# Optimization experiments

Hardware: AMD Instinct MI355X
Metric: run time of the kernel (lower is better)

The kernel has to match this reference:

```python
import jax, jax.numpy as jnp
import numpy as np

N = 30000      # nodes
E = 480000     # edges (before self-loops)
IN = 32        # input_dim
H = 8          # heads
C = 64         # hidden_dim (per-head out channels)
HC = H * C     # 512, concat width
L = 3          # num_layers
NEG_SLOPE = 0.2  # PyG GATConv default


def setup_inputs() -> dict:
    key = jax.random.key(0)
    ks = jax.random.split(key, 16)
    s = 0.05
    return {
        "x": jax.random.normal(ks[0], (N, IN), jnp.float32),
        "edge_index": jax.random.randint(ks[1], (2, E), 0, N, jnp.int32),
        # input projection
        "W_in": jax.random.normal(ks[2], (IN, HC), jnp.float32) * s,
        "b_in": jnp.zeros((HC,), jnp.float32),
        # stacked GATConv params (L layers)
        "W_gat": jax.random.normal(ks[3], (L, HC, HC), jnp.float32) * s,
        "att_src": jax.random.normal(ks[4], (L, H, C), jnp.float32) * s,
        "att_dst": jax.random.normal(ks[5], (L, H, C), jnp.float32) * s,
        "b_gat": jnp.zeros((L, HC), jnp.float32),
        # heads
        "W_att": jax.random.normal(ks[6], (HC, H), jnp.float32) * s,
        "b_att": jnp.zeros((H,), jnp.float32),
        "W_h1": jax.random.normal(ks[7], (HC, C), jnp.float32) * s,
        "b_h1": jnp.zeros((C,), jnp.float32),
        "W_h2": jax.random.normal(ks[8], (C, 1), jnp.float32) * s,
        "b_h2": jnp.zeros((1,), jnp.float32),
    }


def _gat_layer(h, src, dst, W, a_src, a_dst, b):
    # h: [N, HC]; src/dst: [E'] (with self-loops)
    hp = (h @ W).reshape(N, H, C)                       # per-head features
    s = jnp.einsum('nhc,hc->nh', hp, a_src)             # [N, H]
    d = jnp.einsum('nhc,hc->nh', hp, a_dst)             # [N, H]
    e = jax.nn.leaky_relu(s[src] + d[dst], NEG_SLOPE)   # [E', H]
    # segment softmax over destination neighborhoods
    m = jax.ops.segment_max(e, dst, num_segments=N)     # [N, H]
    ex = jnp.exp(e - m[dst])
    den = jax.ops.segment_sum(ex, dst, num_segments=N)
    alpha = ex / (den[dst] + 1e-16)                     # [E', H]
    msg = hp[src] * alpha[:, :, None]                   # [E', H, C]
    out = jax.ops.segment_sum(msg, dst, num_segments=N).reshape(N, HC) + b
    return out


def reference(x, edge_index, W_in, b_in, W_gat, att_src, att_dst, b_gat,
              W_att, b_att, W_h1, b_h1, W_h2, b_h2):
    # PyG GATConv adds self-loops by default
    loops = jnp.arange(N, dtype=edge_index.dtype)
    src = jnp.concatenate([edge_index[0], loops])
    dst = jnp.concatenate([edge_index[1], loops])

    h = jax.nn.relu(x @ W_in + b_in)                    # input_proj + ReLU
    for l in range(L):
        h = jax.nn.relu(_gat_layer(h, src, dst, W_gat[l], att_src[l], att_dst[l], b_gat[l]))
        # dropout is identity in eval mode
    attention_weights = jax.nn.softmax(h @ W_att + b_att, axis=1)   # [N, H]
    anomaly_scores = jax.nn.sigmoid(jax.nn.relu(h @ W_h1 + b_h1) @ W_h2 + b_h2)  # [N, 1]
    return (anomaly_scores, attention_weights)
```

## Files before the change

### kernel.cpp

```cpp
#include <hip/hip_runtime.h>
#include <hip/hip_bf16.h>
#include <math.h>

#define HCW 512
#define NHD 8
#define CCH 64

typedef unsigned short u16;
typedef unsigned int   u32;
typedef __attribute__((ext_vector_type(8))) short bf16x8;
typedef __attribute__((ext_vector_type(4))) float f32x4;

__device__ __forceinline__ float bf2f(u32 u) {
  union { float f; u32 i; } v; v.i = u << 16; return v.f;
}
__device__ __forceinline__ u16 f2bf(float f) {
  u32 x = __builtin_bit_cast(u32, f);
  return (u16)((x + 0x7fff + ((x >> 16) & 1)) >> 16);
}
__device__ __forceinline__ void gload_lds16(const void* g, void* l) {
  __builtin_amdgcn_global_load_lds(
      (const __attribute__((address_space(1))) u32*)g,
      (__attribute__((address_space(3))) u32*)l, 16, 0, 0);
}

__global__ void k_hist(const int* __restrict__ ei, int* __restrict__ deg, int E, int N) {
  int e = blockIdx.x * blockDim.x + threadIdx.x;
  if (e >= E + N) return;
  int dst = (e < E) ? ei[E + e] : (e - E);
  atomicAdd(&deg[dst], 1);
}

__global__ __launch_bounds__(256) void k_scan1(const int* __restrict__ deg, int* __restrict__ ptr,
                                               int* __restrict__ bsum, int n) {
  __shared__ int sm[256];
  int b = blockIdx.x, i = b * 256 + threadIdx.x;
  int v = (i < n) ? deg[i] : 0;
  sm[threadIdx.x] = v;
  __syncthreads();
  for (int off = 1; off < 256; off <<= 1) {
    int t = (threadIdx.x >= off) ? sm[threadIdx.x - off] : 0;
    __syncthreads();
    sm[threadIdx.x] += t;
    __syncthreads();
  }
  if (i < n) ptr[i + 1] = sm[threadIdx.x];
  if (threadIdx.x == 255) bsum[b] = sm[255];
}

__global__ __launch_bounds__(256) void k_scan2(const int* __restrict__ bsum, int* __restrict__ boff, int nb) {
  __shared__ int sm[256];
  int v = (threadIdx.x < nb) ? bsum[threadIdx.x] : 0;
  sm[threadIdx.x] = v;
  __syncthreads();
  for (int off = 1; off < 256; off <<= 1) {
    int t = (threadIdx.x >= off) ? sm[threadIdx.x - off] : 0;
    __syncthreads();
    sm[threadIdx.x] += t;
    __syncthreads();
  }
  if (threadIdx.x < nb) boff[threadIdx.x] = sm[threadIdx.x] - v;
}

__global__ __launch_bounds__(256) void k_scan3(int* __restrict__ ptr, const int* __restrict__ boff, int n) {
  int i = blockIdx.x * 256 + threadIdx.x;
  if (i == 0) ptr[0] = 0;
  if (i < n) ptr[i + 1] += boff[blockIdx.x];
}

__global__ void k_fill(const int* __restrict__ ei, const int* __restrict__ ptr,
                       int* __restrict__ cnt, int* __restrict__ csr_src, int E, int N) {
  int e = blockIdx.x * blockDim.x + threadIdx.x;
  if (e >= E + N) return;
  int src, dst;
  if (e < E) { src = ei[e]; dst = ei[E + e]; } else { src = e - E; dst = e - E; }
  int pos = ptr[dst] + atomicAdd(&cnt[dst], 1);
  csr_src[pos] = src;
}

__global__ __launch_bounds__(256) void k_wconv(const float* __restrict__ W, u16* __restrict__ Wt) {
  __shared__ float sm[32][33];
  int l = blockIdx.z;
  int k0 = blockIdx.y * 32, n0 = blockIdx.x * 32;
  const float* Wl = W + (size_t)l * HCW * HCW;
  u16* Wtl = Wt + (size_t)l * HCW * HCW;
  int tx = threadIdx.x & 31, ty = threadIdx.x >> 5;
  #pragma unroll
  for (int r = 0; r < 32; r += 8)
    sm[ty + r][tx] = Wl[(size_t)(k0 + ty + r) * HCW + n0 + tx];
  __syncthreads();
  #pragma unroll
  for (int r = 0; r < 32; r += 8)
    Wtl[(size_t)(n0 + ty + r) * HCW + k0 + tx] = f2bf(sm[tx][ty + r]);
}

__global__ __launch_bounds__(256) void k_wfconv(const float* __restrict__ W_h1,
                                                const float* __restrict__ W_att,
                                                u16* __restrict__ Wf) {
  int n = blockIdx.x;
  for (int k = threadIdx.x; k < 512; k += 256) {
    float v = 0.f;
    if (n < 64) v = W_h1[(size_t)k * 64 + n];
    else if (n < 72) v = W_att[(size_t)k * 8 + (n - 64)];
    Wf[(size_t)n * 512 + k] = f2bf(v);
  }
}

__global__ __launch_bounds__(256) void k_xconv(const float* __restrict__ x, u16* __restrict__ xb, int total) {
  int i = (blockIdx.x * 256 + threadIdx.x) * 8;
  if (i >= total) return;
  float4 a = *(const float4*)(x + i);
  float4 b = *(const float4*)(x + i + 4);
  uint4 o;
  o.x = (u32)f2bf(a.x) | ((u32)f2bf(a.y) << 16);
  o.y = (u32)f2bf(a.z) | ((u32)f2bf(a.w) << 16);
  o.z = (u32)f2bf(b.x) | ((u32)f2bf(b.y) << 16);
  o.w = (u32)f2bf(b.z) | ((u32)f2bf(b.w) << 16);
  *(uint4*)(xb + i) = o;
}

__global__ __launch_bounds__(256) void k_winconv(const float* __restrict__ W, u16* __restrict__ Wt) {
  int idx = blockIdx.x * 256 + threadIdx.x;
  int n = idx >> 5, k = idx & 31;
  Wt[idx] = f2bf(W[(size_t)k * HCW + n]);
}

__global__ __launch_bounds__(256) void k_inproj3(const u16* __restrict__ xb, const u16* __restrict__ Wt,
                                                 const float* __restrict__ b, u16* __restrict__ h, int N) {
  __shared__ u16 As[128 * 32];
  __shared__ u16 Bs[128 * 32];
  int tid = threadIdx.x, lane = tid & 63, w = tid >> 6;
  int bm = blockIdx.y * 128, bn = blockIdx.x * 128;
  #pragma unroll
  for (int it = 0; it < 4; it++) {
    int g = it * 256 + tid;
    if (g < 512) {
      int row = g >> 2, gb = g & 3, gs = gb ^ (row & 3);
      int ar = bm + row; if (ar >= N) ar = N - 1;
      gload_lds16(xb + (size_t)ar * 32 + gs * 8, &As[g * 8]);
    } else {
      int gg = g - 512;
      int row = gg >> 2, gb = gg & 3, gs = gb ^ (row & 3);
      gload_lds16(Wt + (size_t)(bn + row) * 32 + gs * 8, &Bs[gg * 8]);
    }
  }
  __syncthreads();
  bf16x8 af[2];
  #pragma unroll
  for (int i = 0; i < 2; i++) {
    int rowA = w * 32 + i * 16 + (lane & 15);
    int gA = (lane >> 4) ^ (rowA & 3);
    af[i] = *(const bf16x8*)&As[rowA * 32 + gA * 8];
  }
  f32x4 acc[2][8] = {};
  #pragma unroll
  for (int j = 0; j < 8; j++) {
    int rowB = j * 16 + (lane & 15);
    int gB = (lane >> 4) ^ (rowB & 3);
    bf16x8 bfr = *(const bf16x8*)&Bs[rowB * 32 + gB * 8];
    #pragma unroll
    for (int i = 0; i < 2; i++)
      acc[i][j] = __builtin_amdgcn_mfma_f32_16x16x32_bf16(af[i], bfr, acc[i][j], 0, 0, 0);
  }
  #pragma unroll
  for (int j = 0; j < 8; j++) {
    int col = bn + j * 16 + (lane & 15);
    float bb = b[col];
    #pragma unroll
    for (int i = 0; i < 2; i++) {
      #pragma unroll
      for (int r = 0; r < 4; r++) {
        int n = bm + w * 32 + i * 16 + (lane >> 4) * 4 + r;
        if (n < N) h[(size_t)n * HCW + col] = f2bf(fmaxf(acc[i][j][r] + bb, 0.f));
      }
    }
  }
}

__global__ __launch_bounds__(256) void k_gemm_mfma(const u16* __restrict__ A,
                                                   const u16* __restrict__ Bt,
                                                   u16* __restrict__ C,
                                                   const float* __restrict__ a_src,
                                                   const float* __restrict__ a_dst,
                                                   float* __restrict__ sarr,
                                                   float* __restrict__ darr,
                                                   int M) {
  __shared__ u16 As[128 * 64];
  __shared__ u16 Bs[128 * 64];
  int tid = threadIdx.x;
  int lane = tid & 63, w = tid >> 6;
  int wr = w >> 1, wc = w & 1;
  int bm = blockIdx.y * 128, bn = blockIdx.x * 128;
  f32x4 acc[4][4] = {};
  for (int k0 = 0; k0 < 512; k0 += 64) {
    __syncthreads();
    #pragma unroll
    for (int it = 0; it < 4; it++) {
      int g = it * 256 + tid;
      int row = g >> 3;
      int gb = g & 7;
      int gs = gb ^ (row & 7);
      int ar = bm + row; if (ar >= M) ar = M - 1;
      gload_lds16(A + (size_t)ar * HCW + k0 + gs * 8, &As[g * 8]);
      gload_lds16(Bt + (size_t)(bn + row) * HCW + k0 + gs * 8, &Bs[g * 8]);
    }
    __syncthreads();
    #pragma unroll
    for (int ks = 0; ks < 2; ks++) {
      bf16x8 af[4], bfr[4];
      #pragma unroll
      for (int f = 0; f < 4; f++) {
        int rowA = wr * 64 + f * 16 + (lane & 15);
        int gA = ((ks * 4 + (lane >> 4)) ^ (rowA & 7));
        af[f] = *(const bf16x8*)&As[rowA * 64 + gA * 8];
        int rowB = wc * 64 + f * 16 + (lane & 15);
        int gB = ((ks * 4 + (lane >> 4)) ^ (rowB & 7));
        bfr[f] = *(const bf16x8*)&Bs[rowB * 64 + gB * 8];
      }
      #pragma unroll
      for (int i = 0; i < 4; i++)
        #pragma unroll
        for (int j = 0; j < 4; j++)
          acc[i][j] = __builtin_amdgcn_mfma_f32_16x16x32_bf16(af[i], bfr[j], acc[i][j], 0, 0, 0);
    }
  }
  int gr_base = bm + wr * 64;
  int gc_base = bn + wc * 64;
  #pragma unroll
  for (int i = 0; i < 4; i++) {
    #pragma unroll
    for (int j = 0; j < 4; j++) {
      int col = gc_base + j * 16 + (lane & 15);
      #pragma unroll
      for (int r = 0; r < 4; r++) {
        int rowg = gr_base + i * 16 + (lane >> 4) * 4 + r;
        if (rowg < M) C[(size_t)rowg * HCW + col] = f2bf(acc[i][j][r]);
      }
    }
  }
  int head = (bn >> 6) + wc;
  float asv[4], adv[4];
  #pragma unroll
  for (int j = 0; j < 4; j++) {
    asv[j] = a_src[head * 64 + j * 16 + (lane & 15)];
    adv[j] = a_dst[head * 64 + j * 16 + (lane & 15)];
  }
  #pragma unroll
  for (int i = 0; i < 4; i++) {
    #pragma unroll
    for (int r = 0; r < 4; r++) {
      float sv = acc[i][0][r] * asv[0] + acc[i][1][r] * asv[1]
               + acc[i][2][r] * asv[2] + acc[i][3][r] * asv[3];
      float dv = acc[i][0][r] * adv[0] + acc[i][1][r] * adv[1]
               + acc[i][2][r] * adv[2] + acc[i][3][r] * adv[3];
      sv += __shfl_xor(sv, 1); dv += __shfl_xor(dv, 1);
      sv += __shfl_xor(sv, 2); dv += __shfl_xor(dv, 2);
      sv += __shfl_xor(sv, 4); dv += __shfl_xor(dv, 4);
      sv += __shfl_xor(sv, 8); dv += __shfl_xor(dv, 8);
      if ((lane & 15) == 0) {
        int rowg = gr_base + i * 16 + (lane >> 4) * 4 + r;
        if (rowg < M) {
          sarr[(size_t)rowg * NHD + head] = sv;
          darr[(size_t)rowg * NHD + head] = dv;
        }
      }
    }
  }
}

__global__ __launch_bounds__(256) void k_alpha(const int* __restrict__ ptr, const int* __restrict__ csr_src,
                                               const float* __restrict__ s, const float* __restrict__ d,
                                               u16* __restrict__ alpha, int N) {
  int wv = threadIdx.x >> 6, lane = threadIdx.x & 63;
  int n = blockIdx.x * 4 + wv;
  if (n >= N) return;
  int hd = lane & 7, g = lane >> 3;
  int beg = ptr[n], end = ptr[n + 1];
  float dn = d[(size_t)n * NHD + hd];
  float den = 0.f;
  for (int i = beg + g; i < end; i += 8) {
    float e = s[(size_t)csr_src[i] * NHD + hd] + dn;
    e = (e > 0.f) ? e : 0.2f * e;
    den += __expf(e);
  }
  den += __shfl_xor(den, 8);
  den += __shfl_xor(den, 16);
  den += __shfl_xor(den, 32);
  float inv = 1.f / (den + 1e-16f);
  for (int i = beg + g; i < end; i += 8) {
    float e = s[(size_t)csr_src[i] * NHD + hd] + dn;
    e = (e > 0.f) ? e : 0.2f * e;
    alpha[(size_t)i * NHD + hd] = f2bf(__expf(e) * inv);
  }
}

__global__ __launch_bounds__(256) void k_agg4(const int* __restrict__ ptr, const int* __restrict__ csr_src,
                                              const u16* __restrict__ hp, const u16* __restrict__ alpha,
                                              const float* __restrict__ bias,
                                              u16* __restrict__ hout, int N) {
  int wv = threadIdx.x >> 6, lane = threadIdx.x & 63;
  int n = blockIdx.x * 4 + wv;
  if (n >= N) return;
  int hd = lane >> 3;
  int c = lane * 8;
  int beg = ptr[n], end = ptr[n + 1];
  float acc[8] = {0.f, 0.f, 0.f, 0.f, 0.f, 0.f, 0.f, 0.f};

  int i = beg;
  for (; i + 8 <= end; i += 8) {
    int sidx[8];
    u32 aw[8];
    uint4 v[8];
    #pragma unroll
    for (int u = 0; u < 8; u++) sidx[u] = csr_src[i + u];
    #pragma unroll
    for (int u = 0; u < 8; u++) aw[u] = alpha[(size_t)(i + u) * NHD + hd];
    #pragma unroll
    for (int u = 0; u < 8; u++) v[u] = *(const uint4*)(hp + (size_t)sidx[u] * HCW + c);
    #pragma unroll
    for (int u = 0; u < 8; u++) {
      float a = bf2f(aw[u]);
      u32 w0 = v[u].x, w1 = v[u].y, w2 = v[u].z, w3 = v[u].w;
      acc[0] += a * bf2f(w0 & 0xffff); acc[1] += a * bf2f(w0 >> 16);
      acc[2] += a * bf2f(w1 & 0xffff); acc[3] += a * bf2f(w1 >> 16);
      acc[4] += a * bf2f(w2 & 0xffff); acc[5] += a * bf2f(w2 >> 16);
      acc[6] += a * bf2f(w3 & 0xffff); acc[7] += a * bf2f(w3 >> 16);
    }
  }
  for (; i < end; i++) {
    int s0 = csr_src[i];
    u32 aw = alpha[(size_t)i * NHD + hd];
    uint4 v0 = *(const uint4*)(hp + (size_t)s0 * HCW + c);
    float a = bf2f(aw);
    u32 w0 = v0.x, w1 = v0.y, w2 = v0.z, w3 = v0.w;
    acc[0] += a * bf2f(w0 & 0xffff); acc[1] += a * bf2f(w0 >> 16);
    acc[2] += a * bf2f(w1 & 0xffff); acc[3] += a * bf2f(w1 >> 16);
    acc[4] += a * bf2f(w2 & 0xffff); acc[5] += a * bf2f(w2 >> 16);
    acc[6] += a * bf2f(w3 & 0xffff); acc[7] += a * bf2f(w3 >> 16);
  }

  float4 bv0 = *(const float4*)(bias + c);
  float4 bv1 = *(const float4*)(bias + c + 4);
  float bb[8] = {bv0.x, bv0.y, bv0.z, bv0.w, bv1.x, bv1.y, bv1.z, bv1.w};
  u32 out[4];
  #pragma unroll
  for (int j = 0; j < 4; j++) {
    float o0 = fmaxf(acc[2 * j] + bb[2 * j], 0.f);
    float o1 = fmaxf(acc[2 * j + 1] + bb[2 * j + 1], 0.f);
    out[j] = (u32)f2bf(o0) | ((u32)f2bf(o1) << 16);
  }
  *(uint4*)(hout + (size_t)n * HCW + c) = make_uint4(out[0], out[1], out[2], out[3]);
}

__global__ __launch_bounds__(256) void k_final2(const u16* __restrict__ A,
                                                const u16* __restrict__ Wf,
                                                const float* __restrict__ b_att,
                                                const float* __restrict__ b_h1,
                                                const float* __restrict__ W_h2,
                                                const float* __restrict__ b_h2,
                                                float* __restrict__ anomaly, float* __restrict__ attw,
                                                int M) {
  __shared__ u16 As[128 * 64];
  __shared__ u16 Bs[80 * 64];
  __shared__ float so[4][32][84];
  int tid = threadIdx.x;
  int lane = tid & 63, w = tid >> 6;
  int bm = blockIdx.x * 128;
  f32x4 acc[2][5] = {};
  for (int k0 = 0; k0 < 512; k0 += 64) {
    __syncthreads();
    #pragma unroll
    for (int it = 0; it < 7; it++) {
      int g = it * 256 + tid;
      if (g < 1024) {
        int row = g >> 3, gb = g & 7;
        int gs = gb ^ (row & 7);
        int ar = bm + row; if (ar >= M) ar = M - 1;
        gload_lds16(A + (size_t)ar * HCW + k0 + gs * 8, &As[g * 8]);
      } else if (g < 1664) {
        int gg = g - 1024;
        int row = gg >> 3, gb = gg & 7;
        int gs = gb ^ (row & 7);
        gload_lds16(Wf + (size_t)row * 512 + k0 + gs * 8, &Bs[gg * 8]);
      }
    }
    __syncthreads();
    #pragma unroll
    for (int ks = 0; ks < 2; ks++) {
      bf16x8 af[2], bfr[5];
      #pragma unroll
      for (int i = 0; i < 2; i++) {
        int rowA = w * 32 + i * 16 + (lane & 15);
        int gA = ((ks * 4 + (lane >> 4)) ^ (rowA & 7));
        af[i] = *(const bf16x8*)&As[rowA * 64 + gA * 8];
      }
      #pragma unroll
      for (int j = 0; j < 5; j++) {
        int rowB = j * 16 + (lane & 15);
        int gB = ((ks * 4 + (lane >> 4)) ^ (rowB & 7));
        bfr[j] = *(const bf16x8*)&Bs[rowB * 64 + gB * 8];
      }
      #pragma unroll
      for (int i = 0; i < 2; i++)
        #pragma unroll
        for (int j = 0; j < 5; j++)
          acc[i][j] = __builtin_amdgcn_mfma_f32_16x16x32_bf16(af[i], bfr[j], acc[i][j], 0, 0, 0);
    }
  }
  #pragma unroll
  for (int i = 0; i < 2; i++) {
    #pragma unroll
    for (int j = 0; j < 5; j++) {
      int col = j * 16 + (lane & 15);
      #pragma unroll
      for (int r = 0; r < 4; r++) {
        int row_l = i * 16 + (lane >> 4) * 4 + r;
        so[w][row_l][col] = acc[i][j][r];
      }
    }
  }
  int row_l = lane >> 1, half = lane & 1;
  int n = bm + w * 32 + row_l;
  if (n < M) {
    float hacc = 0.f;
    #pragma unroll
    for (int kk = 0; kk < 32; kk++) {
      int cc = half * 32 + kk;
      float v = fmaxf(so[w][row_l][cc] + b_h1[cc], 0.f);
      hacc += v * W_h2[cc];
    }
    hacc += __shfl_xor(hacc, 1);
    if (half == 0) {
      anomaly[n] = 1.f / (1.f + __expf(-(hacc + b_h2[0])));
    } else {
      float lg[8];
      float mx = -1e30f;
      #pragma unroll
      for (int j = 0; j < 8; j++) {
        lg[j] = so[w][row_l][64 + j] + b_att[j];
        mx = fmaxf(mx, lg[j]);
      }
      float sum = 0.f;
      #pragma unroll
      for (int j = 0; j < 8; j++) { lg[j] = __expf(lg[j] - mx); sum += lg[j]; }
      float inv = 1.f / sum;
      #pragma unroll
      for (int j = 0; j < 8; j++) attw[(size_t)n * 8 + j] = lg[j] * inv;
    }
  }
}

extern "C" void kernel_launch(void* const* d_in, const int* in_sizes, int n_in,
                              void* d_out, int out_size, void* d_ws, size_t ws_size,
                              hipStream_t stream) {
  const float* x       = (const float*)d_in[0];
  const int*   ei      = (const int*)d_in[1];
  const float* W_in    = (const float*)d_in[2];
  const float* b_in    = (const float*)d_in[3];
  const float* W_gat   = (const float*)d_in[4];
  const float* att_src = (const float*)d_in[5];
  const float* att_dst = (const float*)d_in[6];
  const float* b_gat   = (const float*)d_in[7];
  const float* W_att   = (const float*)d_in[8];
  const float* b_att   = (const float*)d_in[9];
  const float* W_h1    = (const float*)d_in[10];
  const float* b_h1    = (const float*)d_in[11];
  const float* W_h2    = (const float*)d_in[12];
  const float* b_h2    = (const float*)d_in[13];

  const int N  = in_sizes[0] / 32;
  const int E  = in_sizes[1] / 2;
  const int ET = E + N;

  char* ws = (char*)d_ws;
  size_t off = 0;
  auto alloc = [&](size_t bytes) -> void* {
    void* p = ws + off;
    off = (off + bytes + 255) & ~(size_t)255;
    return p;
  };
  u16* h     = (u16*)alloc((size_t)N * HCW * 2);
  u16* hp    = (u16*)alloc((size_t)N * HCW * 2);
  u16* Wt    = (u16*)alloc((size_t)3 * HCW * HCW * 2);
  u16* Wf    = (u16*)alloc((size_t)80 * 512 * 2);
  u16* xb    = (u16*)alloc((size_t)N * 32 * 2);
  u16* Wtin  = (u16*)alloc((size_t)512 * 32 * 2);
  u16* alpha = (u16*)alloc((size_t)ET * NHD * 2);
  float* sarr = (float*)alloc((size_t)N * NHD * 4);
  float* darr = (float*)alloc((size_t)N * NHD * 4);
  int* deg    = (int*)alloc((size_t)N * 4);
  int* ptr    = (int*)alloc((size_t)(N + 1) * 4);
  int* cnt    = (int*)alloc((size_t)N * 4);
  int* csr    = (int*)alloc((size_t)ET * 4);
  int* bsum   = (int*)alloc((size_t)1024 * 4);
  int* boff   = (int*)alloc((size_t)1024 * 4);

  float* anomaly = (float*)d_out;
  float* attw    = (float*)d_out + N;

  hipMemsetAsync(deg, 0, (size_t)N * 4, stream);
  hipMemsetAsync(cnt, 0, (size_t)N * 4, stream);

  int gbE = (ET + 255) / 256;
  int nb  = (N + 255) / 256;
  k_hist<<<gbE, 256, 0, stream>>>(ei, deg, E, N);
  k_scan1<<<nb, 256, 0, stream>>>(deg, ptr, bsum, N);
  k_scan2<<<1, 256, 0, stream>>>(bsum, boff, nb);
  k_scan3<<<nb, 256, 0, stream>>>(ptr, boff, N);
  k_fill<<<gbE, 256, 0, stream>>>(ei, ptr, cnt, csr, E, N);

  k_wconv<<<dim3(16, 16, 3), 256, 0, stream>>>(W_gat, Wt);
  k_wfconv<<<80, 256, 0, stream>>>(W_h1, W_att, Wf);
  k_xconv<<<(N * 32 / 8 + 255) / 256, 256, 0, stream>>>(x, xb, N * 32);
  k_winconv<<<64, 256, 0, stream>>>(W_in, Wtin);
  k_inproj3<<<dim3(4, (N + 127) / 128), 256, 0, stream>>>(xb, Wtin, b_in, h, N);

  dim3 ggrid(HCW / 128, (N + 127) / 128);
  for (int l = 0; l < 3; l++) {
    k_gemm_mfma<<<ggrid, 256, 0, stream>>>(h, Wt + (size_t)l * HCW * HCW, hp,
                                           att_src + (size_t)l * NHD * CCH,
                                           att_dst + (size_t)l * NHD * CCH,
                                           sarr, darr, N);
    k_alpha<<<(N + 3) / 4, 256, 0, stream>>>(ptr, csr, sarr, darr, alpha, N);
    k_agg4<<<(N + 3) / 4, 256, 0, stream>>>(ptr, csr, hp, alpha,
                                            b_gat + (size_t)l * HCW, h, N);
  }

  k_final2<<<(N + 127) / 128, 256, 0, stream>>>(h, Wf, b_att, b_h1, W_h2, b_h2,
                                                anomaly, attw, N);
}
```

Before: 483.2 us.

## Fuse softmax into aggregation, replace scan with atomic alloc, merge prep kernels, XCD-swizzle GEMM

```diff
diff --git a/kernel.cpp b/kernel.cpp
--- a/kernel.cpp
+++ b/kernel.cpp
@@ -31,98 +31,81 @@
   atomicAdd(&deg[dst], 1);
 }
 
-__global__ __launch_bounds__(256) void k_scan1(const int* __restrict__ deg, int* __restrict__ ptr,
-                                               int* __restrict__ bsum, int n) {
-  __shared__ int sm[256];
-  int b = blockIdx.x, i = b * 256 + threadIdx.x;
-  int v = (i < n) ? deg[i] : 0;
-  sm[threadIdx.x] = v;
-  __syncthreads();
-  for (int off = 1; off < 256; off <<= 1) {
-    int t = (threadIdx.x >= off) ? sm[threadIdx.x - off] : 0;
-    __syncthreads();
-    sm[threadIdx.x] += t;
-    __syncthreads();
-  }
-  if (i < n) ptr[i + 1] = sm[threadIdx.x];
-  if (threadIdx.x == 255) bsum[b] = sm[255];
-}
-
-__global__ __launch_bounds__(256) void k_scan2(const int* __restrict__ bsum, int* __restrict__ boff, int nb) {
-  __shared__ int sm[256];
-  int v = (threadIdx.x < nb) ? bsum[threadIdx.x] : 0;
-  sm[threadIdx.x] = v;
-  __syncthreads();
-  for (int off = 1; off < 256; off <<= 1) {
-    int t = (threadIdx.x >= off) ? sm[threadIdx.x - off] : 0;
-    __syncthreads();
-    sm[threadIdx.x] += t;
-    __syncthreads();
-  }
-  if (threadIdx.x < nb) boff[threadIdx.x] = sm[threadIdx.x] - v;
-}
-
-__global__ __launch_bounds__(256) void k_scan3(int* __restrict__ ptr, const int* __restrict__ boff, int n) {
-  int i = blockIdx.x * 256 + threadIdx.x;
-  if (i == 0) ptr[0] = 0;
-  if (i < n) ptr[i + 1] += boff[blockIdx.x];
-}
-
-__global__ void k_fill(const int* __restrict__ ei, const int* __restrict__ ptr,
+__global__ __launch_bounds__(256) void k_alloc(const int* __restrict__ deg, int* __restrict__ beg,
+                                               int* __restrict__ cursor, int N) {
+  int n = blockIdx.x * 256 + threadIdx.x;
+  int lane = threadIdx.x & 63;
+  int v = (n < N) ? deg[n] : 0;
+  int incl = v;
+  #pragma unroll
+  for (int off = 1; off < 64; off <<= 1) {
+    int t = __shfl_up(incl, off);
+    if (lane >= off) incl += t;
+  }
+  int total = __shfl(incl, 63);
+  int base = 0;
+  if (lane == 63) base = atomicAdd(cursor, total);
+  base = __shfl(base, 63);
+  if (n < N) beg[n] = base + incl - v;
+}
+
+__global__ void k_fill(const int* __restrict__ ei, const int* __restrict__ beg,
                        int* __restrict__ cnt, int* __restrict__ csr_src, int E, int N) {
   int e = blockIdx.x * blockDim.x + threadIdx.x;
   if (e >= E + N) return;
   int src, dst;
   if (e < E) { src = ei[e]; dst = ei[E + e]; } else { src = e - E; dst = e - E; }
-  int pos = ptr[dst] + atomicAdd(&cnt[dst], 1);
+  int pos = beg[dst] + atomicAdd(&cnt[dst], 1);
   csr_src[pos] = src;
 }
 
-__global__ __launch_bounds__(256) void k_wconv(const float* __restrict__ W, u16* __restrict__ Wt) {
+__global__ __launch_bounds__(256) void k_prep(const float* __restrict__ W_gat, u16* __restrict__ Wt,
+                                              const float* __restrict__ W_h1, const float* __restrict__ W_att,
+                                              u16* __restrict__ Wf,
+                                              const float* __restrict__ x, u16* __restrict__ xb, int xtotal,
+                                              const float* __restrict__ W_in, u16* __restrict__ Wtin,
+                                              int XB) {
   __shared__ float sm[32][33];
-  int l = blockIdx.z;
-  int k0 = blockIdx.y * 32, n0 = blockIdx.x * 32;
-  const float* Wl = W + (size_t)l * HCW * HCW;
-  u16* Wtl = Wt + (size_t)l * HCW * HCW;
-  int tx = threadIdx.x & 31, ty = threadIdx.x >> 5;
-  #pragma unroll
-  for (int r = 0; r < 32; r += 8)
-    sm[ty + r][tx] = Wl[(size_t)(k0 + ty + r) * HCW + n0 + tx];
-  __syncthreads();
-  #pragma unroll
-  for (int r = 0; r < 32; r += 8)
-    Wtl[(size_t)(n0 + ty + r) * HCW + k0 + tx] = f2bf(sm[tx][ty + r]);
-}
-
-__global__ __launch_bounds__(256) void k_wfconv(const float* __restrict__ W_h1,
-                                                const float* __restrict__ W_att,
-                                                u16* __restrict__ Wf) {
-  int n = blockIdx.x;
-  for (int k = threadIdx.x; k < 512; k += 256) {
-    float v = 0.f;
-    if (n < 64) v = W_h1[(size_t)k * 64 + n];
-    else if (n < 72) v = W_att[(size_t)k * 8 + (n - 64)];
-    Wf[(size_t)n * 512 + k] = f2bf(v);
-  }
-}
-
-__global__ __launch_bounds__(256) void k_xconv(const float* __restrict__ x, u16* __restrict__ xb, int total) {
-  int i = (blockIdx.x * 256 + threadIdx.x) * 8;
-  if (i >= total) return;
-  float4 a = *(const float4*)(x + i);
-  float4 b = *(const float4*)(x + i + 4);
-  uint4 o;
-  o.x = (u32)f2bf(a.x) | ((u32)f2bf(a.y) << 16);
-  o.y = (u32)f2bf(a.z) | ((u32)f2bf(a.w) << 16);
-  o.z = (u32)f2bf(b.x) | ((u32)f2bf(b.y) << 16);
-  o.w = (u32)f2bf(b.z) | ((u32)f2bf(b.w) << 16);
-  *(uint4*)(xb + i) = o;
-}
-
-__global__ __launch_bounds__(256) void k_winconv(const float* __restrict__ W, u16* __restrict__ Wt) {
-  int idx = blockIdx.x * 256 + threadIdx.x;
-  int n = idx >> 5, k = idx & 31;
-  Wt[idx] = f2bf(W[(size_t)k * HCW + n]);
+  int b = blockIdx.x;
+  int t = threadIdx.x;
+  if (b < 768) {
+    int l = b >> 8, rem = b & 255;
+    int n0 = (rem & 15) * 32, k0 = (rem >> 4) * 32;
+    const float* Wl = W_gat + (size_t)l * HCW * HCW;
+    u16* Wtl = Wt + (size_t)l * HCW * HCW;
+    int tx = t & 31, ty = t >> 5;
+    #pragma unroll
+    for (int r = 0; r < 32; r += 8)
+      sm[ty + r][tx] = Wl[(size_t)(k0 + ty + r) * HCW + n0 + tx];
+    __syncthreads();
+    #pragma unroll
+    for (int r = 0; r < 32; r += 8)
+      Wtl[(size_t)(n0 + ty + r) * HCW + k0 + tx] = f2bf(sm[tx][ty + r]);
+  } else if (b < 848) {
+    int n = b - 768;
+    for (int k = t; k < 512; k += 256) {
+      float v = 0.f;
+      if (n < 64) v = W_h1[(size_t)k * 64 + n];
+      else if (n < 72) v = W_att[(size_t)k * 8 + (n - 64)];
+      Wf[(size_t)n * 512 + k] = f2bf(v);
+    }
+  } else if (b < 848 + XB) {
+    int i = ((b - 848) * 256 + t) * 8;
+    if (i < xtotal) {
+      float4 a = *(const float4*)(x + i);
+      float4 bb = *(const float4*)(x + i + 4);
+      uint4 o;
+      o.x = (u32)f2bf(a.x) | ((u32)f2bf(a.y) << 16);
+      o.y = (u32)f2bf(a.z) | ((u32)f2bf(a.w) << 16);
+      o.z = (u32)f2bf(bb.x) | ((u32)f2bf(bb.y) << 16);
+      o.w = (u32)f2bf(bb.z) | ((u32)f2bf(bb.w) << 16);
+      *(uint4*)(xb + i) = o;
+    }
+  } else {
+    int idx = (b - 848 - XB) * 256 + t;
+    int n = idx >> 5, k = idx & 31;
+    Wtin[idx] = f2bf(W_in[(size_t)k * HCW + n]);
+  }
 }
 
 __global__ __launch_bounds__(256) void k_inproj3(const u16* __restrict__ xb, const u16* __restrict__ Wt,
@@ -185,12 +168,21 @@
                                                    float* __restrict__ sarr,
                                                    float* __restrict__ darr,
                                                    int M) {
+  int nPanels = (M + 127) >> 7;
+  int lin = blockIdx.y * 4 + blockIdx.x;
+  int xcd = lin & 7;
+  int t = lin >> 3;
+  int bn_i = t & 3;
+  int p = t >> 2;
+  int bm_i = p * 8 + xcd;
+  if (bm_i >= nPanels) return;
+  int bm = bm_i * 128, bn = bn_i * 128;
+
   __shared__ u16 As[128 * 64];
   __shared__ u16 Bs[128 * 64];
   int tid = threadIdx.x;
   int lane = tid & 63, w = tid >> 6;
   int wr = w >> 1, wc = w & 1;
-  int bm = blockIdx.y * 128, bn = blockIdx.x * 128;
   f32x4 acc[4][4] = {};
   for (int k0 = 0; k0 < 512; k0 += 64) {
     __syncthreads();
@@ -268,58 +260,38 @@
   }
 }
 
-__global__ __launch_bounds__(256) void k_alpha(const int* __restrict__ ptr, const int* __restrict__ csr_src,
-                                               const float* __restrict__ s, const float* __restrict__ d,
-                                               u16* __restrict__ alpha, int N) {
-  int wv = threadIdx.x >> 6, lane = threadIdx.x & 63;
-  int n = blockIdx.x * 4 + wv;
-  if (n >= N) return;
-  int hd = lane & 7, g = lane >> 3;
-  int beg = ptr[n], end = ptr[n + 1];
-  float dn = d[(size_t)n * NHD + hd];
-  float den = 0.f;
-  for (int i = beg + g; i < end; i += 8) {
-    float e = s[(size_t)csr_src[i] * NHD + hd] + dn;
-    e = (e > 0.f) ? e : 0.2f * e;
-    den += __expf(e);
-  }
-  den += __shfl_xor(den, 8);
-  den += __shfl_xor(den, 16);
-  den += __shfl_xor(den, 32);
-  float inv = 1.f / (den + 1e-16f);
-  for (int i = beg + g; i < end; i += 8) {
-    float e = s[(size_t)csr_src[i] * NHD + hd] + dn;
-    e = (e > 0.f) ? e : 0.2f * e;
-    alpha[(size_t)i * NHD + hd] = f2bf(__expf(e) * inv);
-  }
-}
-
-__global__ __launch_bounds__(256) void k_agg4(const int* __restrict__ ptr, const int* __restrict__ csr_src,
-                                              const u16* __restrict__ hp, const u16* __restrict__ alpha,
-                                              const float* __restrict__ bias,
+__global__ __launch_bounds__(256) void k_agg7(const int* __restrict__ beg_, const int* __restrict__ deg_,
+                                              const int* __restrict__ csr_src,
+                                              const u16* __restrict__ hp, const float* __restrict__ s,
+                                              const float* __restrict__ d, const float* __restrict__ bias,
                                               u16* __restrict__ hout, int N) {
   int wv = threadIdx.x >> 6, lane = threadIdx.x & 63;
   int n = blockIdx.x * 4 + wv;
   if (n >= N) return;
   int hd = lane >> 3;
   int c = lane * 8;
-  int beg = ptr[n], end = ptr[n + 1];
+  int beg = beg_[n], end = beg + deg_[n];
+  float dn = d[(size_t)n * NHD + hd];
   float acc[8] = {0.f, 0.f, 0.f, 0.f, 0.f, 0.f, 0.f, 0.f};
+  float den = 0.f;
 
   int i = beg;
   for (; i + 8 <= end; i += 8) {
     int sidx[8];
-    u32 aw[8];
+    #pragma unroll
+    for (int u = 0; u < 8; u++) sidx[u] = csr_src[i + u];
+    float ev[8];
+    #pragma unroll
+    for (int u = 0; u < 8; u++) ev[u] = s[(size_t)sidx[u] * NHD + hd] + dn;
     uint4 v[8];
     #pragma unroll
-    for (int u = 0; u < 8; u++) sidx[u] = csr_src[i + u];
-    #pragma unroll
-    for (int u = 0; u < 8; u++) aw[u] = alpha[(size_t)(i + u) * NHD + hd];
-    #pragma unroll
     for (int u = 0; u < 8; u++) v[u] = *(const uint4*)(hp + (size_t)sidx[u] * HCW + c);
     #pragma unroll
     for (int u = 0; u < 8; u++) {
-      float a = bf2f(aw[u]);
+      float e = ev[u];
+      e = (e > 0.f) ? e : 0.2f * e;
+      float a = __expf(e);
+      den += a;
       u32 w0 = v[u].x, w1 = v[u].y, w2 = v[u].z, w3 = v[u].w;
       acc[0] += a * bf2f(w0 & 0xffff); acc[1] += a * bf2f(w0 >> 16);
       acc[2] += a * bf2f(w1 & 0xffff); acc[3] += a * bf2f(w1 >> 16);
@@ -329,9 +301,11 @@
   }
   for (; i < end; i++) {
     int s0 = csr_src[i];
-    u32 aw = alpha[(size_t)i * NHD + hd];
+    float e = s[(size_t)s0 * NHD + hd] + dn;
     uint4 v0 = *(const uint4*)(hp + (size_t)s0 * HCW + c);
-    float a = bf2f(aw);
+    e = (e > 0.f) ? e : 0.2f * e;
+    float a = __expf(e);
+    den += a;
     u32 w0 = v0.x, w1 = v0.y, w2 = v0.z, w3 = v0.w;
     acc[0] += a * bf2f(w0 & 0xffff); acc[1] += a * bf2f(w0 >> 16);
     acc[2] += a * bf2f(w1 & 0xffff); acc[3] += a * bf2f(w1 >> 16);
@@ -339,14 +313,15 @@
     acc[6] += a * bf2f(w3 & 0xffff); acc[7] += a * bf2f(w3 >> 16);
   }
 
+  float inv = 1.f / (den + 1e-16f);
   float4 bv0 = *(const float4*)(bias + c);
   float4 bv1 = *(const float4*)(bias + c + 4);
   float bb[8] = {bv0.x, bv0.y, bv0.z, bv0.w, bv1.x, bv1.y, bv1.z, bv1.w};
   u32 out[4];
   #pragma unroll
   for (int j = 0; j < 4; j++) {
-    float o0 = fmaxf(acc[2 * j] + bb[2 * j], 0.f);
-    float o1 = fmaxf(acc[2 * j + 1] + bb[2 * j + 1], 0.f);
+    float o0 = fmaxf(acc[2 * j] * inv + bb[2 * j], 0.f);
+    float o1 = fmaxf(acc[2 * j + 1] * inv + bb[2 * j + 1], 0.f);
     out[j] = (u32)f2bf(o0) | ((u32)f2bf(o1) << 16);
   }
   *(uint4*)(hout + (size_t)n * HCW + c) = make_uint4(out[0], out[1], out[2], out[3]);
@@ -485,44 +460,41 @@
   u16* Wf    = (u16*)alloc((size_t)80 * 512 * 2);
   u16* xb    = (u16*)alloc((size_t)N * 32 * 2);
   u16* Wtin  = (u16*)alloc((size_t)512 * 32 * 2);
-  u16* alpha = (u16*)alloc((size_t)ET * NHD * 2);
   float* sarr = (float*)alloc((size_t)N * NHD * 4);
   float* darr = (float*)alloc((size_t)N * NHD * 4);
-  int* deg    = (int*)alloc((size_t)N * 4);
-  int* ptr    = (int*)alloc((size_t)(N + 1) * 4);
-  int* cnt    = (int*)alloc((size_t)N * 4);
+  int* zbuf   = (int*)alloc((size_t)(2 * N + 64) * 4);
+  int* deg    = zbuf;
+  int* cnt    = zbuf + N;
+  int* cursor = zbuf + 2 * N;
+  int* beg    = (int*)alloc((size_t)N * 4);
   int* csr    = (int*)alloc((size_t)ET * 4);
-  int* bsum   = (int*)alloc((size_t)1024 * 4);
-  int* boff   = (int*)alloc((size_t)1024 * 4);
 
   float* anomaly = (float*)d_out;
   float* attw    = (float*)d_out + N;
 
-  hipMemsetAsync(deg, 0, (size_t)N * 4, stream);
-  hipMemsetAsync(cnt, 0, (size_t)N * 4, stream);
+  hipMemsetAsync(zbuf, 0, (size_t)(2 * N + 1) * 4, stream);
 
   int gbE = (ET + 255) / 256;
   int nb  = (N + 255) / 256;
   k_hist<<<gbE, 256, 0, stream>>>(ei, deg, E, N);
-  k_scan1<<<nb, 256, 0, stream>>>(deg, ptr, bsum, N);
-  k_scan2<<<1, 256, 0, stream>>>(bsum, boff, nb);
-  k_scan3<<<nb, 256, 0, stream>>>(ptr, boff, N);
-  k_fill<<<gbE, 256, 0, stream>>>(ei, ptr, cnt, csr, E, N);
-
-  k_wconv<<<dim3(16, 16, 3), 256, 0, stream>>>(W_gat, Wt);
-  k_wfconv<<<80, 256, 0, stream>>>(W_h1, W_att, Wf);
-  k_xconv<<<(N * 32 / 8 + 255) / 256, 256, 0, stream>>>(x, xb, N * 32);
-  k_winconv<<<64, 256, 0, stream>>>(W_in, Wtin);
+  k_alloc<<<nb, 256, 0, stream>>>(deg, beg, cursor, N);
+  k_fill<<<gbE, 256, 0, stream>>>(ei, beg, cnt, csr, E, N);
+
+  int xtotal = N * 32;
+  int XB = (xtotal / 8 + 255) / 256;
+  k_prep<<<848 + XB + 64, 256, 0, stream>>>(W_gat, Wt, W_h1, W_att, Wf, x, xb, xtotal,
+                                            W_in, Wtin, XB);
   k_inproj3<<<dim3(4, (N + 127) / 128), 256, 0, stream>>>(xb, Wtin, b_in, h, N);
 
-  dim3 ggrid(HCW / 128, (N + 127) / 128);
+  int nPanels = (N + 127) / 128;
+  int nPanelsPad = ((nPanels + 7) / 8) * 8;
+  dim3 ggrid(4, nPanelsPad);
   for (int l = 0; l < 3; l++) {
     k_gemm_mfma<<<ggrid, 256, 0, stream>>>(h, Wt + (size_t)l * HCW * HCW, hp,
                                            att_src + (size_t)l * NHD * CCH,
                                            att_dst + (size_t)l * NHD * CCH,
                                            sarr, darr, N);
-    k_alpha<<<(N + 3) / 4, 256, 0, stream>>>(ptr, csr, sarr, darr, alpha, N);
-    k_agg4<<<(N + 3) / 4, 256, 0, stream>>>(ptr, csr, hp, alpha,
+    k_agg7<<<(N + 3) / 4, 256, 0, stream>>>(beg, deg, csr, hp, sarr, darr,
                                             b_gat + (size_t)l * HCW, h, N);
   }
 
```

Measured after the change: 431.1 us. 10.8% less time.
